# Performance work log

Hardware: AMD Instinct MI355X
Metric: run time of the kernel (lower is better)

Reference implementation:

```python
import jax, jax.numpy as jnp
import numpy as np

C = 1.0                 # ball curvature magnitude (k = -c)
SQRT_C = float(np.sqrt(C))
MIN_NORM = 1e-15
BALL_EPS = 4e-3         # geoopt float32 projection eps


def _artanh(x):
    return jnp.arctanh(jnp.clip(x, -1.0 + 1e-7, 1.0 - 1e-7))


def _norm(x):
    return jnp.clip(jnp.linalg.norm(x, axis=-1, keepdims=True), MIN_NORM)


def expmap0(u):
    n = _norm(u)
    return jnp.tanh(SQRT_C * n) * u / (SQRT_C * n)


def logmap0(y):
    n = _norm(y)
    return _artanh(SQRT_C * n) * y / (SQRT_C * n)


def mobius_add(x, y):
    x2 = jnp.sum(x * x, axis=-1, keepdims=True)
    y2 = jnp.sum(y * y, axis=-1, keepdims=True)
    xy = jnp.sum(x * y, axis=-1, keepdims=True)
    num = (1.0 + 2.0 * C * xy + C * y2) * x + (1.0 - C * x2) * y
    den = 1.0 + 2.0 * C * xy + C * C * x2 * y2
    return num / jnp.clip(den, MIN_NORM)


def mobius_matvec(W, x):
    # x: [N, in], W: [out, in]
    mx = x @ W.T                                   # [N, out]
    xn = _norm(x)
    mxn = _norm(mx)
    res = jnp.tanh(mxn / xn * _artanh(SQRT_C * xn)) * mx / (mxn * SQRT_C)
    zero = jnp.linalg.norm(mx, axis=-1, keepdims=True) <= 1e-10
    return jnp.where(zero, jnp.zeros_like(res), res)


def project(x):
    n = _norm(x)
    maxnorm = (1.0 - BALL_EPS) / SQRT_C
    return jnp.where(n > maxnorm, x * (maxnorm / n), x)


def setup_inputs() -> dict:
    key = jax.random.key(0)
    k1, k2, k3, k4, k5 = jax.random.split(key, 5)
    N, E, D_IN, D_OUT = 100000, 600000, 128, 128
    x_h = jax.random.normal(k1, (N, D_IN), dtype=jnp.float32) * 0.05  # inside ball
    edge_index = jax.random.randint(k2, (2, E), 0, N, dtype=jnp.int64)
    edge_weight = jax.random.uniform(k3, (E,), dtype=jnp.float32)
    xav = float(np.sqrt(2.0 / (D_IN + D_OUT)))
    W = jax.random.normal(k4, (D_OUT, D_IN), dtype=jnp.float32) * xav
    b = jax.random.normal(k5, (D_OUT,), dtype=jnp.float32) * 0.01
    a = jnp.asarray(0.25, dtype=jnp.float32)  # PReLU slope
    return {"x_h": x_h, "edge_index": edge_index, "edge_weight": edge_weight,
            "W": W, "b": b, "a": a}


def reference(x_h, edge_index, edge_weight, W, b, a):
    N = x_h.shape[0]
    # HyperbolicLinear: mobius matvec + mobius bias add
    h = mobius_matvec(W, x_h)
    h = mobius_add(h, expmap0(b))
    # tangent-space aggregation
    h_t = logmap0(h)                                  # [N, D]
    src, dst = edge_index[0], edge_index[1]
    msg = h_t[src] * edge_weight[:, None]             # [E, D]
    agg = jax.ops.segment_sum(msg, dst, num_segments=N) + h_t
    # mobius PReLU activation
    h2_t = logmap0(expmap0(agg))
    h2_t = jnp.where(h2_t >= 0, h2_t, a * h2_t)
    return project(expmap0(h2_t))
```

## Files before the change

### kernel.cpp

```cpp
#include <hip/hip_runtime.h>
#include <hip/hip_fp16.h>
#include <cstdint>

#define D 128
#define BLK 256

constexpr float MINN    = 1e-15f;
constexpr float ATCLIP  = 1.0f - 1e-7f;
constexpr float BALLEPS = 4e-3f;

typedef _Float16 f16x8 __attribute__((ext_vector_type(8)));
typedef float    f32x4 __attribute__((ext_vector_type(4)));

union H4 { _Float16 h[4]; uint2 u2; };
union H8 { _Float16 h[8]; uint4 u4; };

typedef __attribute__((address_space(1))) const void gas_v;
typedef __attribute__((address_space(3))) void las_v;

__device__ __forceinline__ float red64(float v) {
    v += __shfl_xor(v, 1, 64);
    v += __shfl_xor(v, 2, 64);
    v += __shfl_xor(v, 4, 64);
    v += __shfl_xor(v, 8, 64);
    v += __shfl_xor(v, 16, 64);
    v += __shfl_xor(v, 32, 64);
    return v;
}

__device__ __forceinline__ int red64i(int v) {
    v += __shfl_xor(v, 1, 64);
    v += __shfl_xor(v, 2, 64);
    v += __shfl_xor(v, 4, 64);
    v += __shfl_xor(v, 8, 64);
    v += __shfl_xor(v, 16, 64);
    v += __shfl_xor(v, 32, 64);
    return v;
}

__device__ __forceinline__ float red16(float v) {
    v += __shfl_xor(v, 1, 64);
    v += __shfl_xor(v, 2, 64);
    v += __shfl_xor(v, 4, 64);
    v += __shfl_xor(v, 8, 64);
    return v;
}

__device__ __forceinline__ float tanh_fast(float x) {
    float e = __expf(2.f * fminf(x, 15.f));
    return __fdividef(e - 1.f, e + 1.f);
}
__device__ __forceinline__ float artanh_fast(float x) {
    x = fminf(x, ATCLIP);
    return 0.5f * __logf(__fdividef(1.f + x, 1.f - x));
}

__global__ __launch_bounds__(256) void k_prep(const float* __restrict__ W,
                                              _Float16* __restrict__ Wh,
                                              int* __restrict__ zero, int zeroInts)
{
    const int t = threadIdx.x;
    const int bid = blockIdx.x;
    if (bid < 8) {
        int i = bid * 256 + t;
        int f = i >> 7;
        int r = i & 127;
        const float4* src = (const float4*)(W + r * 128 + f * 8);
        float4 v0 = src[0], v1 = src[1];
        H8 u;
        u.h[0] = (_Float16)v0.x; u.h[1] = (_Float16)v0.y;
        u.h[2] = (_Float16)v0.z; u.h[3] = (_Float16)v0.w;
        u.h[4] = (_Float16)v1.x; u.h[5] = (_Float16)v1.y;
        u.h[6] = (_Float16)v1.z; u.h[7] = (_Float16)v1.w;
        *(uint4*)(Wh + i * 8) = u.u4;
    } else {
        int i = (bid - 8) * 256 + t;
        int base = i * 4;
        if (base + 3 < zeroInts) {
            *(int4*)(zero + base) = make_int4(0, 0, 0, 0);
        } else if (base < zeroInts) {
            for (int k = base; k < zeroInts; ++k) zero[k] = 0;
        }
    }
}

__global__ __launch_bounds__(BLK) void k_node_mfma(
    const float* __restrict__ x, const _Float16* __restrict__ Wh,
    const float* __restrict__ b, uint2* __restrict__ ht, int N,
    const int* __restrict__ ei, int* __restrict__ cnt,
    int* __restrict__ rank, int E, int eslice, int use_rank)
{
    __shared__ float xs[64 * 128];

    const int t     = threadIdx.x;
    const int lane  = t & 63;
    const int w     = t >> 6;
    const int node0 = blockIdx.x * 128;
    const int e0    = blockIdx.x * eslice;

    int ed[4];
#pragma unroll
    for (int k = 0; k < 4; ++k) {
        int idx = min(e0 + k * BLK + t, E - 1);
        ed[k] = ei[E + idx];
    }
    __builtin_amdgcn_sched_barrier(0);

    float2 b2 = ((const float2*)b)[lane];
    __builtin_amdgcn_sched_barrier(0);

#pragma unroll
    for (int i = 0; i < 8; ++i) {
        int P      = (w * 8 + i) * 64 + lane;
        int node   = P >> 5;
        int q      = (P & 31) ^ (node & 7);
        int node_g = min(node0 + node, N - 1);
        const float* src = x + (size_t)node_g * 128 + q * 4;
        char* dst = (char*)xs + (size_t)(w * 8 + i) * 1024;
        __builtin_amdgcn_global_load_lds((gas_v*)src, (las_v*)dst, 16, 0, 0);
    }
    __builtin_amdgcn_sched_barrier(0);

    f32x4 rv[8];
#pragma unroll
    for (int i = 0; i < 8; ++i) {
        int P      = (w * 8 + i) * 64 + lane;
        int node   = P >> 5;
        int q      = (P & 31) ^ (node & 7);
        int node_g = min(node0 + 64 + node, N - 1);
        rv[i] = *(const f32x4*)(x + (size_t)node_g * 128 + q * 4);
    }
    __builtin_amdgcn_sched_barrier(0);

    float pb  = fmaf(b2.x, b2.x, b2.y * b2.y);
    float bn2 = red64(pb);
    float bnc    = fmaxf(sqrtf(bn2), MINN);
    float bscale = __fdividef(tanh_fast(bnc), bnc);
    const float y2 = bscale * bscale * bn2;

    const int c = lane & 15;
    const int g = lane >> 4;
    const int bnode = w * 16 + c;
    const int sw    = bnode & 7;
    const float* xrow = &xs[bnode * 128];
    const float4* b4  = (const float4*)b;
    uint2* lout = (uint2*)((char*)xs + (size_t)w * 8192);

    auto do_tile = [&](int tb) {
        f32x4 Cf[8];
#pragma unroll
        for (int mt = 0; mt < 8; ++mt) Cf[mt] = (f32x4){0.f, 0.f, 0.f, 0.f};
        float px = 0.f;

#pragma unroll
        for (int s = 0; s < 4; ++s) {
            int q0 = s * 8 + g * 2;
            f32x4 lo = *(const f32x4*)&xrow[(q0 ^ sw) * 4];
            f32x4 hi = *(const f32x4*)&xrow[((q0 + 1) ^ sw) * 4];
            px = fmaf(lo[0], lo[0], px); px = fmaf(lo[1], lo[1], px);
            px = fmaf(lo[2], lo[2], px); px = fmaf(lo[3], lo[3], px);
            px = fmaf(hi[0], hi[0], px); px = fmaf(hi[1], hi[1], px);
            px = fmaf(hi[2], hi[2], px); px = fmaf(hi[3], hi[3], px);
            f16x8 Bf;
            Bf[0] = (_Float16)lo[0]; Bf[1] = (_Float16)lo[1];
            Bf[2] = (_Float16)lo[2]; Bf[3] = (_Float16)lo[3];
            Bf[4] = (_Float16)hi[0]; Bf[5] = (_Float16)hi[1];
            Bf[6] = (_Float16)hi[2]; Bf[7] = (_Float16)hi[3];
            const _Float16* wp = Wh + ((s * 4 + g) << 10) + (c << 3);
#pragma unroll
            for (int mt = 0; mt < 8; ++mt) {
                f16x8 Af = *(const f16x8*)&wp[mt << 7];
                Cf[mt] = __builtin_amdgcn_mfma_f32_16x16x32_f16(Af, Bf, Cf[mt], 0, 0, 0);
            }
        }

        float pm = 0.f, pdb = 0.f;
#pragma unroll
        for (int mt = 0; mt < 8; ++mt) {
            float4 bv = b4[mt * 4 + g];
            pm  = fmaf(Cf[mt][0], Cf[mt][0], pm);
            pm  = fmaf(Cf[mt][1], Cf[mt][1], pm);
            pm  = fmaf(Cf[mt][2], Cf[mt][2], pm);
            pm  = fmaf(Cf[mt][3], Cf[mt][3], pm);
            pdb = fmaf(Cf[mt][0], bv.x, pdb);
            pdb = fmaf(Cf[mt][1], bv.y, pdb);
            pdb = fmaf(Cf[mt][2], bv.z, pdb);
            pdb = fmaf(Cf[mt][3], bv.w, pdb);
        }
        float xn2 = px;
        xn2 += __shfl_xor(xn2, 16); xn2 += __shfl_xor(xn2, 32);
        pm  += __shfl_xor(pm, 16);  pm  += __shfl_xor(pm, 32);
        pdb += __shfl_xor(pdb, 16); pdb += __shfl_xor(pdb, 32);
        float pd = bscale * pdb;

        float xn      = fmaxf(sqrtf(xn2), MINN);
        float mxn_raw = sqrtf(pm);
        float mxn     = fmaxf(mxn_raw, MINN);
        float alpha   = __fdividef(tanh_fast(__fdividef(mxn, xn) * artanh_fast(xn)), mxn);
        if (mxn_raw <= 1e-10f) alpha = 0.f;

        float x2  = alpha * alpha * pm;
        float xy  = alpha * pd;
        float den = fmaxf(fmaf(x2, y2, 1.f + 2.f * xy), MINN);
        float ca  = __fdividef((1.f + 2.f * xy + y2) * alpha, den);
        float cb  = __fdividef(1.f - x2, den);

        float hn2 = ca * ca * pm + 2.f * ca * cb * pd + cb * cb * y2;
        float hn  = fmaxf(sqrtf(hn2), MINN);
        float lsc = __fdividef(artanh_fast(hn), hn);
        float s1  = lsc * ca;
        float s2b = lsc * cb * bscale;

#pragma unroll
        for (int mt = 0; mt < 8; ++mt) {
            float4 bv = b4[mt * 4 + g];
            H4 u;
            u.h[0] = (_Float16)fmaf(s1, Cf[mt][0], s2b * bv.x);
            u.h[1] = (_Float16)fmaf(s1, Cf[mt][1], s2b * bv.y);
            u.h[2] = (_Float16)fmaf(s1, Cf[mt][2], s2b * bv.z);
            u.h[3] = (_Float16)fmaf(s1, Cf[mt][3], s2b * bv.w);
            lout[c * 33 + mt * 4 + g] = u.u2;
        }
    };

    auto copyout = [&](int tb) {
#pragma unroll
        for (int it = 0; it < 8; ++it) {
            int lin  = it * BLK + t;
            int node = lin >> 5;
            int col  = lin & 31;
            int gn   = tb + node;
            if (gn < N) {
                const uint2* lsrc = (const uint2*)((const char*)xs + (size_t)(node >> 4) * 8192);
                ht[(size_t)gn * 32 + col] = lsrc[(node & 15) * 33 + col];
            }
        }
    };

    asm volatile("s_waitcnt vmcnt(8)" ::: "memory");
    __builtin_amdgcn_sched_barrier(0);

    do_tile(node0);
    __syncthreads();
    copyout(node0);

    asm volatile("s_waitcnt lgkmcnt(0)" ::: "memory");
    __builtin_amdgcn_sched_barrier(0);
    __builtin_amdgcn_s_barrier();
    __builtin_amdgcn_sched_barrier(0);

#pragma unroll
    for (int i = 0; i < 8; ++i) {
        float* dst = (float*)((char*)xs + (size_t)(w * 8 + i) * 1024 + (size_t)lane * 16);
        *(f32x4*)dst = rv[i];
    }

    do_tile(node0 + 64);
    __syncthreads();
    copyout(node0 + 64);

#pragma unroll
    for (int k = 0; k < 4; ++k) {
        int i = k * BLK + t;
        int e = e0 + i;
        if (i < eslice && e < E) {
            int r = atomicAdd(&cnt[ed[k]], 1);
            if (use_rank) rank[e] = r;
        }
    }
    for (int i = 4 * BLK + t; i < eslice; i += BLK) {
        int e = e0 + i;
        if (e < E) {
            int r = atomicAdd(&cnt[ei[E + e]], 1);
            if (use_rank) rank[e] = r;
        }
    }
}

__global__ __launch_bounds__(256) void k_scan(
    const int* __restrict__ cnt, int* __restrict__ ptr,
    unsigned long long* __restrict__ lb, int N)
{
    __shared__ int s[256];
    __shared__ int sbase;
    const int t   = threadIdx.x;
    const int bid = blockIdx.x;
    const int lane = t & 63;
    const int w    = t >> 6;

    int base = bid * 1024 + t * 4;
    int v0 = 0, v1 = 0, v2 = 0, v3 = 0;
    if (base + 3 < N) {
        int4 q = *(const int4*)&cnt[base];
        v0 = q.x; v1 = q.y; v2 = q.z; v3 = q.w;
    } else {
        if (base + 0 < N) v0 = cnt[base + 0];
        if (base + 1 < N) v1 = cnt[base + 1];
        if (base + 2 < N) v2 = cnt[base + 2];
        if (base + 3 < N) v3 = cnt[base + 3];
    }
    int sum = v0 + v1 + v2 + v3;
    s[t] = sum;
    __syncthreads();
    for (int off = 1; off < 256; off <<= 1) {
        int xv = (t >= off) ? s[t - off] : 0;
        __syncthreads();
        s[t] += xv;
        __syncthreads();
    }
    int excl  = s[t] - sum;
    int total = s[255];

    if (t == 255) {
        unsigned long long pkt =
            ((unsigned long long)((bid == 0) ? 2u : 1u) << 32) | (unsigned)total;
        __hip_atomic_store(&lb[bid], pkt, __ATOMIC_RELEASE, __HIP_MEMORY_SCOPE_AGENT);
        if (bid == 0) sbase = 0;
    }

    if (bid > 0 && w == 3) {
        int exclb = 0;
        int j = bid - 1;
        while (true) {
            int idx = j - lane;
            unsigned f = 0; int v = 0;
            if (idx >= 0) {
                unsigned long long p;
                do {
                    p = __hip_atomic_load(&lb[idx], __ATOMIC_ACQUIRE, __HIP_MEMORY_SCOPE_AGENT);
                    f = (unsigned)(p >> 32);
                } while (f == 0);
                v = (int)(unsigned)(p & 0xffffffffu);
            }
            unsigned long long m2 = __ballot(f == 2u);
            if (m2) {
                int Lstop = __ffsll((long long)m2) - 1;
                int contrib = (lane <= Lstop) ? v : 0;
                exclb += red64i(contrib);
                break;
            } else {
                exclb += red64i((idx >= 0) ? v : 0);
                j -= 64;
            }
        }
        if (lane == 0) {
            unsigned long long pkt2 =
                ((unsigned long long)2u << 32) | (unsigned)(exclb + total);
            __hip_atomic_store(&lb[bid], pkt2, __ATOMIC_RELEASE, __HIP_MEMORY_SCOPE_AGENT);
            sbase = exclb;
        }
    }
    __syncthreads();

    int r = excl + sbase;
    if (base + 0 < N) ptr[base + 0] = r; r += v0;
    if (base + 1 < N) ptr[base + 1] = r; r += v1;
    if (base + 2 < N) ptr[base + 2] = r; r += v2;
    if (base + 3 < N) ptr[base + 3] = r;
}

__global__ __launch_bounds__(256) void k_scatter_rank(
    const int* __restrict__ ei, const float* __restrict__ ew,
    const int* __restrict__ ptr, const int* __restrict__ rank,
    int2* __restrict__ sorted, int E)
{
    int e = blockIdx.x * 256 + threadIdx.x;
    if (e >= E) return;
    int src = ei[e];
    int dst = ei[E + e];
    float w = ew[e];
    int pos = ptr[dst] + rank[e];
    sorted[pos] = make_int2(src << 8, __float_as_int(w));
}

__global__ __launch_bounds__(256) void k_scatter_atomic(
    const int* __restrict__ ei, const float* __restrict__ ew,
    int* __restrict__ ptr, int2* __restrict__ sorted, int E)
{
    int e = blockIdx.x * 256 + threadIdx.x;
    if (e >= E) return;
    int src = ei[e];
    int dst = ei[E + e];
    float w = ew[e];
    int pos = atomicAdd(&ptr[dst], 1);
    sorted[pos] = make_int2(src << 8, __float_as_int(w));
}

__global__ __launch_bounds__(256) void k_agg_final(
    const char* __restrict__ htb, const int* __restrict__ ptr,
    const int* __restrict__ cnt, const int2* __restrict__ sorted,
    const float* __restrict__ a_in, float* __restrict__ out, int N, int rmode)
{
    const int t   = threadIdx.x;
    const int li  = t & 15;
    const int grp = t >> 4;
    const int n   = blockIdx.x * 16 + grp;
    if (n >= N) return;
    const float a = a_in[0];

    H8 own; own.u4 = *(const uint4*)(htb + (size_t)n * 256 + li * 16);
    float acc[8];
#pragma unroll
    for (int k = 0; k < 8; ++k) acc[k] = (float)own.h[k];

    int basep = ptr[n];
    int cn    = cnt[n];
    int s0    = rmode ? basep : basep - cn;
    int e0    = s0 + cn;

    const int lioff = li * 16;
    int j = s0;
    for (; j + 4 <= e0; j += 4) {
        int2 d0 = sorted[j];
        int2 d1 = sorted[j + 1];
        int2 d2 = sorted[j + 2];
        int2 d3 = sorted[j + 3];
        H8 g0, g1, g2, g3;
        g0.u4 = *(const uint4*)(htb + (unsigned)d0.x + lioff);
        g1.u4 = *(const uint4*)(htb + (unsigned)d1.x + lioff);
        g2.u4 = *(const uint4*)(htb + (unsigned)d2.x + lioff);
        g3.u4 = *(const uint4*)(htb + (unsigned)d3.x + lioff);
        float w0 = __int_as_float(d0.y);
        float w1 = __int_as_float(d1.y);
        float w2 = __int_as_float(d2.y);
        float w3 = __int_as_float(d3.y);
#pragma unroll
        for (int k = 0; k < 8; ++k) acc[k] = fmaf((float)g0.h[k], w0, acc[k]);
#pragma unroll
        for (int k = 0; k < 8; ++k) acc[k] = fmaf((float)g1.h[k], w1, acc[k]);
#pragma unroll
        for (int k = 0; k < 8; ++k) acc[k] = fmaf((float)g2.h[k], w2, acc[k]);
#pragma unroll
        for (int k = 0; k < 8; ++k) acc[k] = fmaf((float)g3.h[k], w3, acc[k]);
    }
    for (; j < e0; ++j) {
        int2 d = sorted[j];
        H8 g; g.u4 = *(const uint4*)(htb + (unsigned)d.x + lioff);
        float w = __int_as_float(d.y);
#pragma unroll
        for (int k = 0; k < 8; ++k) acc[k] = fmaf((float)g.h[k], w, acc[k]);
    }

    float pv = 0.f;
#pragma unroll
    for (int k = 0; k < 8; ++k) {
        float v = acc[k];
        v = (v >= 0.f) ? v : a * v;
        acc[k] = v;
        pv = fmaf(v, v, pv);
    }
    float m2 = red16(pv);
    float rc = fmaxf(sqrtf(m2), MINN);
    float te = tanh_fast(rc);
    const float maxn = 1.0f - BALLEPS;
    float fsc = __fdividef(fminf(fmaxf(te, MINN), maxn), rc);

    float4 o0 = make_float4(fsc * acc[0], fsc * acc[1], fsc * acc[2], fsc * acc[3]);
    float4 o1 = make_float4(fsc * acc[4], fsc * acc[5], fsc * acc[6], fsc * acc[7]);
    float4* orow = (float4*)(out + (size_t)n * D);
    orow[li * 2 + 0] = o0;
    orow[li * 2 + 1] = o1;
}

extern "C" void kernel_launch(void* const* d_in, const int* in_sizes, int n_in,
                              void* d_out, int out_size, void* d_ws, size_t ws_size,
                              hipStream_t stream)
{
    const float* x  = (const float*)d_in[0];
    const int*   ei = (const int*)  d_in[1];
    const float* ew = (const float*)d_in[2];
    const float* W  = (const float*)d_in[3];
    const float* b  = (const float*)d_in[4];
    const float* a  = (const float*)d_in[5];
    float* out = (float*)d_out;

    const int N = in_sizes[0] / D;
    const int E = in_sizes[1] / 2;
    const int nc = (N + 1023) / 1024;

    char* ws = (char*)d_ws;
    size_t HT_B       = (size_t)N * D * 2;
    uint2*              ht  = (uint2*)ws;
    size_t off_cnt    = HT_B;
    int*                cnt = (int*)(ws + off_cnt);
    size_t off_lb     = (off_cnt + (size_t)N * 4 + 15) & ~(size_t)15;
    unsigned long long* lb  = (unsigned long long*)(ws + off_lb);
    size_t off_ptr    = (off_lb + (size_t)nc * 8 + 15) & ~(size_t)15;
    int*                ptr = (int*)(ws + off_ptr);
    size_t off_sorted = (off_ptr + (size_t)N * 4 + 15) & ~(size_t)15;
    int2*               sorted = (int2*)(ws + off_sorted);
    size_t off_wh     = off_sorted + (size_t)E * 8;
    _Float16*           Wh  = (_Float16*)(ws + off_wh);
    size_t off_rank   = off_wh + 32768;
    int*                rank = (int*)(ws + off_rank);
    int use_rank = (ws_size >= off_rank + (size_t)E * 4) ? 1 : 0;

    int zeroInts = (int)((off_ptr - off_cnt) / 4);
    int zb  = ((zeroInts + 3) / 4 + 255) / 256;
    int nb1 = (N + 127) / 128;
    int eslice = (E + nb1 - 1) / nb1;

    k_prep<<<8 + zb, 256, 0, stream>>>(W, Wh, cnt, zeroInts);
    k_node_mfma<<<nb1, BLK, 0, stream>>>(x, Wh, b, ht, N, ei, cnt,
                                         use_rank ? rank : nullptr, E, eslice, use_rank);
    k_scan<<<nc, 256, 0, stream>>>(cnt, ptr, lb, N);
    if (use_rank)
        k_scatter_rank<<<(E + 255) / 256, 256, 0, stream>>>(ei, ew, ptr, rank, sorted, E);
    else
        k_scatter_atomic<<<(E + 255) / 256, 256, 0, stream>>>(ei, ew, ptr, sorted, E);
    k_agg_final<<<(N + 15) / 16, 256, 0, stream>>>((const char*)ht, ptr, cnt, sorted, a, out, N, use_rank);
}
```

Before: 204.0 us.

## Process one 64-node tile per block and drop register-staged prefetch

The node kernel now handles 64 nodes per block instead of 128, doubling the grid and removing the register-held prefetch of the second tile and the early prefetch of destination indices. Edge counting is done with a plain strided loop that loads indices on demand. The intent is to cut register pressure and raise occupancy and parallelism. The cost is losing the in-block load/compute overlap, and each block must redo the bias-norm setup.

```diff
diff --git a/kernel.cpp b/kernel.cpp
--- a/kernel.cpp
+++ b/kernel.cpp
@@ -93,18 +93,9 @@
     __shared__ float xs[64 * 128];
 
     const int t     = threadIdx.x;
+    const int node0 = blockIdx.x * 64;
     const int lane  = t & 63;
     const int w     = t >> 6;
-    const int node0 = blockIdx.x * 128;
-    const int e0    = blockIdx.x * eslice;
-
-    int ed[4];
-#pragma unroll
-    for (int k = 0; k < 4; ++k) {
-        int idx = min(e0 + k * BLK + t, E - 1);
-        ed[k] = ei[E + idx];
-    }
-    __builtin_amdgcn_sched_barrier(0);
 
     float2 b2 = ((const float2*)b)[lane];
     __builtin_amdgcn_sched_barrier(0);
@@ -121,158 +112,120 @@
     }
     __builtin_amdgcn_sched_barrier(0);
 
-    f32x4 rv[8];
-#pragma unroll
-    for (int i = 0; i < 8; ++i) {
-        int P      = (w * 8 + i) * 64 + lane;
-        int node   = P >> 5;
-        int q      = (P & 31) ^ (node & 7);
-        int node_g = min(node0 + 64 + node, N - 1);
-        rv[i] = *(const f32x4*)(x + (size_t)node_g * 128 + q * 4);
-    }
-    __builtin_amdgcn_sched_barrier(0);
-
     float pb  = fmaf(b2.x, b2.x, b2.y * b2.y);
     float bn2 = red64(pb);
     float bnc    = fmaxf(sqrtf(bn2), MINN);
     float bscale = __fdividef(tanh_fast(bnc), bnc);
     const float y2 = bscale * bscale * bn2;
 
+    asm volatile("s_waitcnt vmcnt(0)" ::: "memory");
+    __builtin_amdgcn_sched_barrier(0);
+
     const int c = lane & 15;
     const int g = lane >> 4;
+
+    f32x4 Cf[8];
+#pragma unroll
+    for (int mt = 0; mt < 8; ++mt) Cf[mt] = (f32x4){0.f, 0.f, 0.f, 0.f};
+
     const int bnode = w * 16 + c;
     const int sw    = bnode & 7;
     const float* xrow = &xs[bnode * 128];
-    const float4* b4  = (const float4*)b;
+    float px = 0.f;
+
+#pragma unroll
+    for (int s = 0; s < 4; ++s) {
+        int q0 = s * 8 + g * 2;
+        f32x4 lo = *(const f32x4*)&xrow[(q0 ^ sw) * 4];
+        f32x4 hi = *(const f32x4*)&xrow[((q0 + 1) ^ sw) * 4];
+        px = fmaf(lo[0], lo[0], px); px = fmaf(lo[1], lo[1], px);
+        px = fmaf(lo[2], lo[2], px); px = fmaf(lo[3], lo[3], px);
+        px = fmaf(hi[0], hi[0], px); px = fmaf(hi[1], hi[1], px);
+        px = fmaf(hi[2], hi[2], px); px = fmaf(hi[3], hi[3], px);
+        f16x8 Bf;
+        Bf[0] = (_Float16)lo[0]; Bf[1] = (_Float16)lo[1];
+        Bf[2] = (_Float16)lo[2]; Bf[3] = (_Float16)lo[3];
+        Bf[4] = (_Float16)hi[0]; Bf[5] = (_Float16)hi[1];
+        Bf[6] = (_Float16)hi[2]; Bf[7] = (_Float16)hi[3];
+        const _Float16* wp = Wh + ((s * 4 + g) << 10) + (c << 3);
+#pragma unroll
+        for (int mt = 0; mt < 8; ++mt) {
+            f16x8 Af = *(const f16x8*)&wp[mt << 7];
+            Cf[mt] = __builtin_amdgcn_mfma_f32_16x16x32_f16(Af, Bf, Cf[mt], 0, 0, 0);
+        }
+    }
+
+    const float4* b4 = (const float4*)b;
+    float pm = 0.f, pdb = 0.f;
+#pragma unroll
+    for (int mt = 0; mt < 8; ++mt) {
+        float4 bv = b4[mt * 4 + g];
+        pm  = fmaf(Cf[mt][0], Cf[mt][0], pm);
+        pm  = fmaf(Cf[mt][1], Cf[mt][1], pm);
+        pm  = fmaf(Cf[mt][2], Cf[mt][2], pm);
+        pm  = fmaf(Cf[mt][3], Cf[mt][3], pm);
+        pdb = fmaf(Cf[mt][0], bv.x, pdb);
+        pdb = fmaf(Cf[mt][1], bv.y, pdb);
+        pdb = fmaf(Cf[mt][2], bv.z, pdb);
+        pdb = fmaf(Cf[mt][3], bv.w, pdb);
+    }
+    float xn2 = px;
+    xn2 += __shfl_xor(xn2, 16); xn2 += __shfl_xor(xn2, 32);
+    pm  += __shfl_xor(pm, 16);  pm  += __shfl_xor(pm, 32);
+    pdb += __shfl_xor(pdb, 16); pdb += __shfl_xor(pdb, 32);
+    float pd = bscale * pdb;
+
+    float xn      = fmaxf(sqrtf(xn2), MINN);
+    float mxn_raw = sqrtf(pm);
+    float mxn     = fmaxf(mxn_raw, MINN);
+    float alpha   = __fdividef(tanh_fast(__fdividef(mxn, xn) * artanh_fast(xn)), mxn);
+    if (mxn_raw <= 1e-10f) alpha = 0.f;
+
+    float x2  = alpha * alpha * pm;
+    float xy  = alpha * pd;
+    float den = fmaxf(fmaf(x2, y2, 1.f + 2.f * xy), MINN);
+    float ca  = __fdividef((1.f + 2.f * xy + y2) * alpha, den);
+    float cb  = __fdividef(1.f - x2, den);
+
+    float hn2 = ca * ca * pm + 2.f * ca * cb * pd + cb * cb * y2;
+    float hn  = fmaxf(sqrtf(hn2), MINN);
+    float lsc = __fdividef(artanh_fast(hn), hn);
+    float s1  = lsc * ca;
+    float s2b = lsc * cb * bscale;
+
     uint2* lout = (uint2*)((char*)xs + (size_t)w * 8192);
-
-    auto do_tile = [&](int tb) {
-        f32x4 Cf[8];
-#pragma unroll
-        for (int mt = 0; mt < 8; ++mt) Cf[mt] = (f32x4){0.f, 0.f, 0.f, 0.f};
-        float px = 0.f;
-
-#pragma unroll
-        for (int s = 0; s < 4; ++s) {
-            int q0 = s * 8 + g * 2;
-            f32x4 lo = *(const f32x4*)&xrow[(q0 ^ sw) * 4];
-            f32x4 hi = *(const f32x4*)&xrow[((q0 + 1) ^ sw) * 4];
-            px = fmaf(lo[0], lo[0], px); px = fmaf(lo[1], lo[1], px);
-            px = fmaf(lo[2], lo[2], px); px = fmaf(lo[3], lo[3], px);
-            px = fmaf(hi[0], hi[0], px); px = fmaf(hi[1], hi[1], px);
-            px = fmaf(hi[2], hi[2], px); px = fmaf(hi[3], hi[3], px);
-            f16x8 Bf;
-            Bf[0] = (_Float16)lo[0]; Bf[1] = (_Float16)lo[1];
-            Bf[2] = (_Float16)lo[2]; Bf[3] = (_Float16)lo[3];
-            Bf[4] = (_Float16)hi[0]; Bf[5] = (_Float16)hi[1];
-            Bf[6] = (_Float16)hi[2]; Bf[7] = (_Float16)hi[3];
-            const _Float16* wp = Wh + ((s * 4 + g) << 10) + (c << 3);
-#pragma unroll
-            for (int mt = 0; mt < 8; ++mt) {
-                f16x8 Af = *(const f16x8*)&wp[mt << 7];
-                Cf[mt] = __builtin_amdgcn_mfma_f32_16x16x32_f16(Af, Bf, Cf[mt], 0, 0, 0);
+#pragma unroll
+    for (int mt = 0; mt < 8; ++mt) {
+        float4 bv = b4[mt * 4 + g];
+        H4 u;
+        u.h[0] = (_Float16)fmaf(s1, Cf[mt][0], s2b * bv.x);
+        u.h[1] = (_Float16)fmaf(s1, Cf[mt][1], s2b * bv.y);
+        u.h[2] = (_Float16)fmaf(s1, Cf[mt][2], s2b * bv.z);
+        u.h[3] = (_Float16)fmaf(s1, Cf[mt][3], s2b * bv.w);
+        lout[c * 33 + mt * 4 + g] = u.u2;
+    }
+    __syncthreads();
+
+    for (int it = 0; it < 8; ++it) {
+        int lin  = it * BLK + t;
+        int node = lin >> 5;
+        int col  = lin & 31;
+        int gn   = node0 + node;
+        if (gn < N) {
+            const uint2* lsrc = (const uint2*)((const char*)xs + (size_t)(node >> 4) * 8192);
+            ht[(size_t)gn * 32 + col] = lsrc[(node & 15) * 33 + col];
+        }
+    }
+
+    __builtin_amdgcn_sched_barrier(0);
+    {
+        int e0 = blockIdx.x * eslice;
+        for (int i = t; i < eslice; i += BLK) {
+            int e = e0 + i;
+            if (e < E) {
+                int r = atomicAdd(&cnt[ei[E + e]], 1);
+                if (use_rank) rank[e] = r;
             }
-        }
-
-        float pm = 0.f, pdb = 0.f;
-#pragma unroll
-        for (int mt = 0; mt < 8; ++mt) {
-            float4 bv = b4[mt * 4 + g];
-            pm  = fmaf(Cf[mt][0], Cf[mt][0], pm);
-            pm  = fmaf(Cf[mt][1], Cf[mt][1], pm);
-            pm  = fmaf(Cf[mt][2], Cf[mt][2], pm);
-            pm  = fmaf(Cf[mt][3], Cf[mt][3], pm);
-            pdb = fmaf(Cf[mt][0], bv.x, pdb);
-            pdb = fmaf(Cf[mt][1], bv.y, pdb);
-            pdb = fmaf(Cf[mt][2], bv.z, pdb);
-            pdb = fmaf(Cf[mt][3], bv.w, pdb);
-        }
-        float xn2 = px;
-        xn2 += __shfl_xor(xn2, 16); xn2 += __shfl_xor(xn2, 32);
-        pm  += __shfl_xor(pm, 16);  pm  += __shfl_xor(pm, 32);
-        pdb += __shfl_xor(pdb, 16); pdb += __shfl_xor(pdb, 32);
-        float pd = bscale * pdb;
-
-        float xn      = fmaxf(sqrtf(xn2), MINN);
-        float mxn_raw = sqrtf(pm);
-        float mxn     = fmaxf(mxn_raw, MINN);
-        float alpha   = __fdividef(tanh_fast(__fdividef(mxn, xn) * artanh_fast(xn)), mxn);
-        if (mxn_raw <= 1e-10f) alpha = 0.f;
-
-        float x2  = alpha * alpha * pm;
-        float xy  = alpha * pd;
-        float den = fmaxf(fmaf(x2, y2, 1.f + 2.f * xy), MINN);
-        float ca  = __fdividef((1.f + 2.f * xy + y2) * alpha, den);
-        float cb  = __fdividef(1.f - x2, den);
-
-        float hn2 = ca * ca * pm + 2.f * ca * cb * pd + cb * cb * y2;
-        float hn  = fmaxf(sqrtf(hn2), MINN);
-        float lsc = __fdividef(artanh_fast(hn), hn);
-        float s1  = lsc * ca;
-        float s2b = lsc * cb * bscale;
-
-#pragma unroll
-        for (int mt = 0; mt < 8; ++mt) {
-            float4 bv = b4[mt * 4 + g];
-            H4 u;
-            u.h[0] = (_Float16)fmaf(s1, Cf[mt][0], s2b * bv.x);
-            u.h[1] = (_Float16)fmaf(s1, Cf[mt][1], s2b * bv.y);
-            u.h[2] = (_Float16)fmaf(s1, Cf[mt][2], s2b * bv.z);
-            u.h[3] = (_Float16)fmaf(s1, Cf[mt][3], s2b * bv.w);
-            lout[c * 33 + mt * 4 + g] = u.u2;
-        }
-    };
-
-    auto copyout = [&](int tb) {
-#pragma unroll
-        for (int it = 0; it < 8; ++it) {
-            int lin  = it * BLK + t;
-            int node = lin >> 5;
-            int col  = lin & 31;
-            int gn   = tb + node;
-            if (gn < N) {
-                const uint2* lsrc = (const uint2*)((const char*)xs + (size_t)(node >> 4) * 8192);
-                ht[(size_t)gn * 32 + col] = lsrc[(node & 15) * 33 + col];
-            }
-        }
-    };
-
-    asm volatile("s_waitcnt vmcnt(8)" ::: "memory");
-    __builtin_amdgcn_sched_barrier(0);
-
-    do_tile(node0);
-    __syncthreads();
-    copyout(node0);
-
-    asm volatile("s_waitcnt lgkmcnt(0)" ::: "memory");
-    __builtin_amdgcn_sched_barrier(0);
-    __builtin_amdgcn_s_barrier();
-    __builtin_amdgcn_sched_barrier(0);
-
-#pragma unroll
-    for (int i = 0; i < 8; ++i) {
-        float* dst = (float*)((char*)xs + (size_t)(w * 8 + i) * 1024 + (size_t)lane * 16);
-        *(f32x4*)dst = rv[i];
-    }
-
-    do_tile(node0 + 64);
-    __syncthreads();
-    copyout(node0 + 64);
-
-#pragma unroll
-    for (int k = 0; k < 4; ++k) {
-        int i = k * BLK + t;
-        int e = e0 + i;
-        if (i < eslice && e < E) {
-            int r = atomicAdd(&cnt[ed[k]], 1);
-            if (use_rank) rank[e] = r;
-        }
-    }
-    for (int i = 4 * BLK + t; i < eslice; i += BLK) {
-        int e = e0 + i;
-        if (e < E) {
-            int r = atomicAdd(&cnt[ei[E + e]], 1);
-            if (use_rank) rank[e] = r;
         }
     }
 }
@@ -497,7 +450,7 @@
 
     int zeroInts = (int)((off_ptr - off_cnt) / 4);
     int zb  = ((zeroInts + 3) / 4 + 255) / 256;
-    int nb1 = (N + 127) / 128;
+    int nb1 = (N + 63) / 64;
     int eslice = (E + nb1 - 1) / nb1;
 
     k_prep<<<8 + zb, 256, 0, stream>>>(W, Wh, cnt, zeroInts);
```

Result: faster. 193.5 us (-5.2%).
